# Performance work log

Measured on AMD Instinct MI355X. Metric: run time of the kernel, lower is better.

Reference implementation:

```python
import jax, jax.numpy as jnp
import numpy as np

H, W = 512, 512
N = H * W
NCLS = 4
D_BI, D_SP = 5, 2
THETA_ALPHA, THETA_BETA, THETA_GAMMA = 80.0, 0.0625, 3.0
BI_COMPAT, SP_COMPAT, COMPATIBILITY = 10.0, 3.0, -1.0
NUM_ITER = 10


def _build_lattice(feats):
    """Permutohedral lattice precompute (numpy, integer index construction).
    feats: [N, d]. Returns os [N,d+1] int32 (1-based), ws [N,d+1] float32,
    bn [d+1, M, 2] int32 (0 = missing neighbor), M."""
    feats = np.asarray(feats, np.float64)
    n, d = feats.shape
    inv_std = np.sqrt(2.0 / 3.0) * (d + 1)
    scale = inv_std / np.sqrt((np.arange(d) + 1.0) * (np.arange(d) + 2.0))
    cf = feats * scale
    # embedding matrix E: elevated = cf @ E.T lies on the hyperplane sum=0
    E = np.zeros((d + 1, d))
    E[0, :] = 1.0
    for j in range(1, d + 1):
        E[j, j:] = 1.0
        E[j, j - 1] = -j
    elevated = cf @ E.T  # [n, d+1]
    greedy = (np.rint(elevated / (d + 1)) * (d + 1)).astype(np.int64)
    diff = elevated - greedy
    idx = np.arange(d + 1)
    upper = idx[None, :] > idx[:, None]
    lower = idx[None, :] < idx[:, None]
    di = diff[:, :, None]
    dj = diff[:, None, :]
    rank = (((dj > di) & upper) | ((dj >= di) & lower)).sum(-1)
    rank = rank + greedy.sum(1, keepdims=True) // (d + 1)
    low = rank < 0
    rank = rank + np.where(low, d + 1, 0)
    greedy = greedy + np.where(low, d + 1, 0)
    high = rank > d
    rank = rank - np.where(high, d + 1, 0)
    greedy = greedy - np.where(high, d + 1, 0)
    # barycentric weights
    bary = np.zeros((n, d + 2))
    v = (elevated - greedy) / (d + 1)
    rows = np.repeat(np.arange(n), d + 1)
    np.add.at(bary, (rows, (d - rank).ravel()), v.ravel())
    np.add.at(bary, (rows, (d + 1 - rank).ravel()), -v.ravel())
    bary[:, 0] += 1.0 + bary[:, d + 1]
    ws = bary[:, : d + 1].astype(np.float32)
    # simplex vertex keys (first d coords; last is implied by zero-sum)
    keys = np.empty((n, d + 1, d), np.int64)
    for r in range(d + 1):
        keys[:, r, :] = (greedy + r - (d + 1) * (rank > d - r))[:, :d]
    flat = keys.reshape(-1, d)
    lo = flat.min(0) - (d + 1)
    hi = flat.max(0) + (d + 1)
    strides = np.cumprod(np.concatenate([[1], (hi - lo + 1)[:-1]]))
    coords = (flat - lo) @ strides
    uniq, first, inv = np.unique(coords, return_index=True, return_inverse=True)
    M = int(len(uniq))
    os_ = (inv.reshape(n, d + 1) + 1).astype(np.int32)
    ukeys = flat[first]
    bn = np.zeros((d + 1, M, 2), np.int32)
    for j in range(d + 1):
        n1 = ukeys - 1
        n2 = ukeys + 1
        if j < d:
            n1[:, j] = ukeys[:, j] + d
            n2[:, j] = ukeys[:, j] - d
        for t, nk in enumerate((n1, n2)):
            c = (nk - lo) @ strides
            pos = np.clip(np.searchsorted(uniq, c), 0, M - 1)
            bn[j, :, t] = np.where(uniq[pos] == c, pos + 1, 0)
    return os_, ws, bn, M


def setup_inputs() -> dict:
    key = jax.random.key(0)
    k1, k2 = jax.random.split(key)
    image = jax.random.uniform(k1, (H, W, 7), dtype=jnp.float32)
    unary = jax.random.normal(k2, (H, W, NCLS), dtype=jnp.float32)
    img = np.asarray(image)
    yy, xx = np.mgrid[0:H, 0:W].astype(np.float64)
    bifeat = np.concatenate(
        [(xx / THETA_ALPHA)[..., None], (yy / THETA_ALPHA)[..., None],
         img[..., :3] / THETA_BETA], axis=-1).reshape(N, D_BI)
    spfeat = np.stack([xx / THETA_GAMMA, yy / THETA_GAMMA], -1).reshape(N, D_SP)
    os_b, ws_b, bn_b, M_b = _build_lattice(bifeat)
    os_s, ws_s, bn_s, M_s = _build_lattice(spfeat)
    return {
        "unary": unary,
        "ws_bilateral": jnp.asarray(ws_b), "os_bilateral": jnp.asarray(os_b),
        "blur_neighbors_bilateral": jnp.asarray(bn_b), "M_bilateral": M_b,
        "ws_spatial": jnp.asarray(ws_s), "os_spatial": jnp.asarray(os_s),
        "blur_neighbors_spatial": jnp.asarray(bn_s), "M_spatial": M_s,
    }


def _perm_filter(values, os_, ws, bn, M, alpha):
    # values: [N, C]; splat -> blur -> slice
    d1 = os_.shape[1]
    C = values.shape[1]
    table = jnp.zeros((M + 1, C), values.dtype)  # row 0 = dummy (missing)
    table = table.at[os_.reshape(-1)].add(
        (values[:, None, :] * ws[:, :, None]).reshape(-1, C))
    for j in range(d1):  # [0.5, 1, 0.5] blur along each lattice axis
        table = table.at[1:].add(0.5 * (table[bn[j, :, 0]] + table[bn[j, :, 1]]))
    return alpha * jnp.einsum("nrc,nr->nc", table[os_], ws)


def _mean_field(unary, ws_b, os_b, bn_b, M_b, ws_s, os_s, bn_s, M_s):
    C = unary.shape[-1]
    u = unary.reshape(N, C)
    alpha_b = 1.0 / (1.0 + 2.0 ** (-D_BI))
    alpha_s = 1.0 / (1.0 + 2.0 ** (-D_SP))
    ones = jnp.ones((N, 1), u.dtype)
    inv_nb = 1.0 / (_perm_filter(ones, os_b, ws_b, bn_b, M_b, alpha_b) + 1e-20)
    inv_ns = 1.0 / (_perm_filter(ones, os_s, ws_s, bn_s, M_s, alpha_s) + 1e-20)
    Q = jax.nn.softmax(-u, axis=-1)
    for _ in range(NUM_ITER):
        msg = (BI_COMPAT * _perm_filter(Q, os_b, ws_b, bn_b, M_b, alpha_b) * inv_nb
               + SP_COMPAT * _perm_filter(Q, os_s, ws_s, bn_s, M_s, alpha_s) * inv_ns)
        Q = jax.nn.softmax(-u - COMPATIBILITY * msg, axis=-1)
    return Q.reshape(H, W, C)


def reference(unary, ws_bilateral, os_bilateral, blur_neighbors_bilateral, M_bilateral,
              ws_spatial, os_spatial, blur_neighbors_spatial, M_spatial):
    # Returns the refined marginals Q [H, W, NCLS]; the module's MAP output is
    # jnp.argmax(Q, -1) (kept soft here so fwd/bwd share one output).
    return _mean_field(unary, ws_bilateral, os_bilateral, blur_neighbors_bilateral,
                       M_bilateral, ws_spatial, os_spatial, blur_neighbors_spatial,
                       M_spatial)
```

## Files before the change

kernel.cpp:

```cpp
#include <hip/hip_runtime.h>

#define NPIX (512 * 512)
#define BLK 256

#define TOTB (NPIX * 6)
#define TOTS (NPIX * 3)
#define TOTE (NPIX * 9)

typedef _Float16 h4 __attribute__((ext_vector_type(4)));
typedef unsigned long long u64;

constexpr float ALPHA_B = 32.0f / 33.0f;
constexpr float ALPHA_S = 0.8f;
constexpr float BI_COMPAT = 10.0f;
constexpr float SP_COMPAT = 3.0f;

__device__ __forceinline__ unsigned pack_ent(int n, float w) {
    float wc = fminf(fmaxf(w, 0.f), 1.f);
    unsigned iw = (unsigned)(wc * 16383.f + 0.5f);
    return (iw << 18) | (unsigned)n;
}
__device__ __forceinline__ int ent_pix(unsigned e) { return (int)(e & 0x3FFFFu); }
__device__ __forceinline__ float ent_w(unsigned e) {
    return (float)(e >> 18) * (1.0f / 16383.0f);
}
__device__ __forceinline__ u64 mknode(int nxt, unsigned pay) {
    return ((u64)(unsigned)nxt << 32) | (u64)pay;
}

__device__ __forceinline__ float4 f4zero() { return make_float4(0.f, 0.f, 0.f, 0.f); }
__device__ __forceinline__ h4 h4zero() {
    h4 z; z.x = (_Float16)0.f; z.y = (_Float16)0.f; z.z = (_Float16)0.f; z.w = (_Float16)0.f;
    return z;
}

__global__ void k_softmax_init(const float4* __restrict__ u, float4* __restrict__ Q) {
    int n = blockIdx.x * BLK + threadIdx.x;
    if (n >= NPIX) return;
    float4 uu = u[n];
    float l0 = -uu.x, l1 = -uu.y, l2 = -uu.z, l3 = -uu.w;
    float m = fmaxf(fmaxf(l0, l1), fmaxf(l2, l3));
    float e0 = expf(l0 - m), e1 = expf(l1 - m), e2 = expf(l2 - m), e3 = expf(l3 - m);
    float inv = 1.0f / (e0 + e1 + e2 + e3);
    Q[n] = make_float4(e0 * inv, e1 * inv, e2 * inv, e3 * inv);
}

template <int D1>
__device__ __forceinline__ void link_slot(const int* __restrict__ os, const float* __restrict__ ws,
                                          int* __restrict__ head, u64* __restrict__ next2,
                                          int n, int r, int obase, int ebase, int lane) {
    int o = obase + os[n * D1 + r];
    int e = ebase + n * D1 + r;
    unsigned pay = pack_ent(n, ws[n * D1 + r]);
    int o_prev = __shfl_up(o, 1);
    bool is_head = (lane == 0) || (o != o_prev);
    u64 hm = __ballot(is_head);
    u64 above = (hm >> lane) >> 1;
    int runlen = above ? __ffsll((long long)above) : (64 - lane);
    int e_prevlane = __shfl_up(e, 1);
    u64 node;
    if (is_head) {
        int e_last = e + (runlen - 1) * D1;
        int old = atomicExch(&head[o], e_last);
        node = mknode(old, pay);
    } else {
        node = mknode(e_prevlane, pay);
    }
    next2[e] = node;
}

__global__ void k_link2_softmax(const int* __restrict__ osb, const float* __restrict__ wsb,
                                const int* __restrict__ oss, const float* __restrict__ wss,
                                int* __restrict__ head, u64* __restrict__ next2,
                                const float4* __restrict__ u, float4* __restrict__ Q,
                                int Vb) {
    int n = blockIdx.x * BLK + threadIdx.x;
    float4 uu = u[n];
    float l0 = -uu.x, l1 = -uu.y, l2 = -uu.z, l3 = -uu.w;
    float m = fmaxf(fmaxf(l0, l1), fmaxf(l2, l3));
    float e0 = expf(l0 - m), e1 = expf(l1 - m), e2 = expf(l2 - m), e3 = expf(l3 - m);
    float inv = 1.0f / (e0 + e1 + e2 + e3);
    Q[n] = make_float4(e0 * inv, e1 * inv, e2 * inv, e3 * inv);
    int lane = threadIdx.x & 63;
#pragma unroll
    for (int r = 0; r < 6; r++) link_slot<6>(osb, wsb, head, next2, n, r, 0, 0, lane);
#pragma unroll
    for (int r = 0; r < 3; r++) link_slot<3>(oss, wss, head, next2, n, r, Vb, TOTB, lane);
}

__global__ void k_compact2(const int* __restrict__ head, const u64* __restrict__ next2,
                           unsigned* __restrict__ ent, int* __restrict__ start,
                           int* __restrict__ endv,
                           float* __restrict__ nB, float* __restrict__ nS,
                           int* __restrict__ cursor, int V, int Vb) {
    __shared__ int lds[BLK];
    __shared__ int sbase;
    int o = blockIdx.x * BLK + threadIdx.x;
    bool valid = o < V;
    int h = valid ? head[o] : -1;
    int len = 0;
    for (int e = h; e >= 0;) { e = (int)(next2[e] >> 32); len++; }
    lds[threadIdx.x] = len;
    __syncthreads();
    for (int off = 1; off < BLK; off <<= 1) {
        int t = ((int)threadIdx.x >= off) ? lds[threadIdx.x - off] : 0;
        __syncthreads();
        lds[threadIdx.x] += t;
        __syncthreads();
    }
    int incl = lds[threadIdx.x];
    if (threadIdx.x == BLK - 1) sbase = atomicAdd(cursor, incl);
    __syncthreads();
    if (!valid) return;
    int pos = sbase + incl - len;
    start[o] = pos;
    endv[o] = pos + len;
    float acc = 0.f;
    for (int e = h; e >= 0;) {
        u64 nd = next2[e];
        unsigned pe = (unsigned)nd;
        acc += ent_w(pe);
        ent[pos++] = pe;
        e = (int)(nd >> 32);
    }
    if (o < Vb) nB[o] = acc;
    else nS[o - Vb] = acc;
}

__global__ void k_link_softmax(const int* __restrict__ osb, const int* __restrict__ oss,
                               int* __restrict__ head, int* __restrict__ next,
                               const float4* __restrict__ u, float4* __restrict__ Q,
                               int Vb) {
    int n = blockIdx.x * BLK + threadIdx.x;
    if (n >= NPIX) return;
    float4 uu = u[n];
    float l0 = -uu.x, l1 = -uu.y, l2 = -uu.z, l3 = -uu.w;
    float m = fmaxf(fmaxf(l0, l1), fmaxf(l2, l3));
    float e0 = expf(l0 - m), e1 = expf(l1 - m), e2 = expf(l2 - m), e3 = expf(l3 - m);
    float inv = 1.0f / (e0 + e1 + e2 + e3);
    Q[n] = make_float4(e0 * inv, e1 * inv, e2 * inv, e3 * inv);
#pragma unroll
    for (int r = 0; r < 6; r++) {
        int o = osb[n * 6 + r];
        int e = n * 6 + r;
        next[e] = atomicExch(&head[o], e);
    }
#pragma unroll
    for (int r = 0; r < 3; r++) {
        int o = Vb + oss[n * 3 + r];
        int e = TOTB + n * 3 + r;
        next[e] = atomicExch(&head[o], e);
    }
}

__global__ void k_compact(const int* __restrict__ head, const int* __restrict__ next,
                          const float* __restrict__ wsb, const float* __restrict__ wss,
                          unsigned* __restrict__ ent, int* __restrict__ start,
                          int* __restrict__ endv,
                          float* __restrict__ nB, float* __restrict__ nS,
                          int* __restrict__ cursor, int V, int Vb) {
    __shared__ int lds[BLK];
    __shared__ int sbase;
    int o = blockIdx.x * BLK + threadIdx.x;
    bool valid = o < V;
    int h = valid ? head[o] : -1;
    int len = 0;
    for (int e = h; e >= 0; e = next[e]) len++;
    lds[threadIdx.x] = len;
    __syncthreads();
    for (int off = 1; off < BLK; off <<= 1) {
        int t = ((int)threadIdx.x >= off) ? lds[threadIdx.x - off] : 0;
        __syncthreads();
        lds[threadIdx.x] += t;
        __syncthreads();
    }
    int incl = lds[threadIdx.x];
    if (threadIdx.x == BLK - 1) sbase = atomicAdd(cursor, incl);
    __syncthreads();
    if (!valid) return;
    int pos = sbase + incl - len;
    start[o] = pos;
    endv[o] = pos + len;
    float acc = 0.f;
    if (o < Vb) {
        for (int e = h; e >= 0; e = next[e]) {
            unsigned n = (unsigned)e / 6u;
            unsigned pe = pack_ent((int)n, wsb[e]);
            acc += ent_w(pe);
            ent[pos++] = pe;
        }
        nB[o] = acc;
    } else {
        for (int e = h; e >= 0; e = next[e]) {
            int ee = e - TOTB;
            unsigned pe = pack_ent(ee / 3, wss[ee]);
            acc += ent_w(pe);
            ent[pos++] = pe;
        }
        nS[o - Vb] = acc;
    }
}

__global__ void k_gather4h_both(const unsigned* __restrict__ ent, const int* __restrict__ start,
                                const int* __restrict__ endv, int V, int Vb,
                                h4* __restrict__ tB, h4* __restrict__ tS,
                                const float4* __restrict__ Q) {
    int i = blockIdx.x * BLK + threadIdx.x;
    if (i >= V) return;
    int s = start[i];
    int e = endv[i];
    float ax = 0.f, ay = 0.f, az = 0.f, aw = 0.f;
    for (int k = s; k < e; k++) {
        unsigned en = ent[k];
        float w = ent_w(en);
        float4 q = Q[ent_pix(en)];
        ax += w * q.x; ay += w * q.y; az += w * q.z; aw += w * q.w;
    }
    h4 h;
    h.x = (_Float16)ax; h.y = (_Float16)ay; h.z = (_Float16)az; h.w = (_Float16)aw;
    if (i < Vb) tB[i] = h;
    else tS[i - Vb] = h;
}

__global__ void k_blur1(const float* __restrict__ in, float* __restrict__ out,
                        const int* __restrict__ bn, int M) {
    int i = blockIdx.x * BLK + threadIdx.x;
    if (i > M) return;
    if (i == 0) { out[0] = 0.f; return; }
    int n1 = bn[(size_t)(i - 1) * 2 + 0];
    int n2 = bn[(size_t)(i - 1) * 2 + 1];
    out[i] = in[i] + 0.5f * (in[n1] + in[n2]);
}

__global__ void k_blur1_both(const float* __restrict__ inB, float* __restrict__ outB,
                             const int* __restrict__ bnB, int Mb,
                             const float* __restrict__ inS, float* __restrict__ outS,
                             const int* __restrict__ bnS, int Ms) {
    int i = blockIdx.x * BLK + threadIdx.x;
    const float* in; float* out; const int* bn; int M, idx;
    if (i <= Mb) { in = inB; out = outB; bn = bnB; M = Mb; idx = i; }
    else {
        idx = i - (Mb + 1);
        if (idx > Ms) return;
        in = inS; out = outS; bn = bnS; M = Ms;
    }
    if (idx == 0) { out[0] = 0.f; return; }
    int n1 = bn[(size_t)(idx - 1) * 2 + 0];
    int n2 = bn[(size_t)(idx - 1) * 2 + 1];
    out[idx] = in[idx] + 0.5f * (in[n1] + in[n2]);
}

__global__ void k_blur4h(const h4* __restrict__ in, h4* __restrict__ out,
                         const int* __restrict__ bn, int M) {
    int i = blockIdx.x * BLK + threadIdx.x;
    if (i > M) return;
    if (i == 0) { out[0] = h4zero(); return; }
    int n1 = bn[(size_t)(i - 1) * 2 + 0];
    int n2 = bn[(size_t)(i - 1) * 2 + 1];
    h4 a = in[i], b = in[n1], c = in[n2];
    h4 o;
    o.x = (_Float16)((float)a.x + 0.5f * ((float)b.x + (float)c.x));
    o.y = (_Float16)((float)a.y + 0.5f * ((float)b.y + (float)c.y));
    o.z = (_Float16)((float)a.z + 0.5f * ((float)b.z + (float)c.z));
    o.w = (_Float16)((float)a.w + 0.5f * ((float)b.w + (float)c.w));
    out[i] = o;
}

__global__ void k_blur4h_both(const h4* __restrict__ inB, h4* __restrict__ outB,
                              const int* __restrict__ bnB, int Mb,
                              const h4* __restrict__ inS, h4* __restrict__ outS,
                              const int* __restrict__ bnS, int Ms) {
    int i = blockIdx.x * BLK + threadIdx.x;
    const h4* in; h4* out; const int* bn; int M, idx;
    if (i <= Mb) { in = inB; out = outB; bn = bnB; M = Mb; idx = i; }
    else {
        idx = i - (Mb + 1);
        if (idx > Ms) return;
        in = inS; out = outS; bn = bnS; M = Ms;
    }
    if (idx == 0) { out[0] = h4zero(); return; }
    int n1 = bn[(size_t)(idx - 1) * 2 + 0];
    int n2 = bn[(size_t)(idx - 1) * 2 + 1];
    h4 a = in[idx], b = in[n1], c = in[n2];
    h4 o;
    o.x = (_Float16)((float)a.x + 0.5f * ((float)b.x + (float)c.x));
    o.y = (_Float16)((float)a.y + 0.5f * ((float)b.y + (float)c.y));
    o.z = (_Float16)((float)a.z + 0.5f * ((float)b.z + (float)c.z));
    o.w = (_Float16)((float)a.w + 0.5f * ((float)b.w + (float)c.w));
    out[idx] = o;
}

__global__ void k_norm_prescale(const float* __restrict__ nTb, const float* __restrict__ wsb,
                                const int* __restrict__ osb,
                                const float* __restrict__ nTs, const float* __restrict__ wss,
                                const int* __restrict__ oss,
                                float* __restrict__ wsbp, float* __restrict__ wssp) {
    int n = blockIdx.x * BLK + threadIdx.x;
    if (n >= NPIX) return;
    float sb = 0.f;
#pragma unroll
    for (int r = 0; r < 6; r++) sb += wsb[n * 6 + r] * nTb[osb[n * 6 + r]];
    float cb = BI_COMPAT * ALPHA_B / (ALPHA_B * sb + 1e-20f);
#pragma unroll
    for (int r = 0; r < 6; r++) wsbp[n * 6 + r] = wsb[n * 6 + r] * cb;
    float ss = 0.f;
#pragma unroll
    for (int r = 0; r < 3; r++) ss += wss[n * 3 + r] * nTs[oss[n * 3 + r]];
    float cs = SP_COMPAT * ALPHA_S / (ALPHA_S * ss + 1e-20f);
#pragma unroll
    for (int r = 0; r < 3; r++) wssp[n * 3 + r] = wss[n * 3 + r] * cs;
}

__global__ void k_slice_combine_h(const float4* __restrict__ u,
                                  const h4* __restrict__ tb, const float* __restrict__ wsbp,
                                  const int* __restrict__ osb,
                                  const h4* __restrict__ ts, const float* __restrict__ wssp,
                                  const int* __restrict__ oss,
                                  float4* __restrict__ Qout) {
    int n = blockIdx.x * BLK + threadIdx.x;
    if (n >= NPIX) return;
    float4 uu = u[n];
    float l0 = -uu.x, l1 = -uu.y, l2 = -uu.z, l3 = -uu.w;
#pragma unroll
    for (int r = 0; r < 6; r++) {
        float w = wsbp[n * 6 + r];
        h4 t = tb[osb[n * 6 + r]];
        l0 += w * (float)t.x; l1 += w * (float)t.y; l2 += w * (float)t.z; l3 += w * (float)t.w;
    }
#pragma unroll
    for (int r = 0; r < 3; r++) {
        float w = wssp[n * 3 + r];
        h4 t = ts[oss[n * 3 + r]];
        l0 += w * (float)t.x; l1 += w * (float)t.y; l2 += w * (float)t.z; l3 += w * (float)t.w;
    }
    float m = fmaxf(fmaxf(l0, l1), fmaxf(l2, l3));
    float e0 = expf(l0 - m), e1 = expf(l1 - m), e2 = expf(l2 - m), e3 = expf(l3 - m);
    float inv = 1.0f / (e0 + e1 + e2 + e3);
    Qout[n] = make_float4(e0 * inv, e1 * inv, e2 * inv, e3 * inv);
}

template <int D1>
__global__ void k_splat1(const float* __restrict__ ws, const int* __restrict__ os,
                         float* __restrict__ table) {
    int n = blockIdx.x * BLK + threadIdx.x;
    if (n >= NPIX) return;
#pragma unroll
    for (int r = 0; r < D1; r++) atomicAdd(&table[os[n * D1 + r]], ws[n * D1 + r]);
}

template <int D1>
__global__ void k_splat4(const float4* __restrict__ Q, const float* __restrict__ ws,
                         const int* __restrict__ os, float* __restrict__ table) {
    int n = blockIdx.x * BLK + threadIdx.x;
    if (n >= NPIX) return;
    float4 q = Q[n];
#pragma unroll
    for (int r = 0; r < D1; r++) {
        float w = ws[n * D1 + r];
        int o = os[n * D1 + r];
        float* t = table + 4 * (size_t)o;
        atomicAdd(t + 0, q.x * w);
        atomicAdd(t + 1, q.y * w);
        atomicAdd(t + 2, q.z * w);
        atomicAdd(t + 3, q.w * w);
    }
}

__global__ void k_blur4(const float4* __restrict__ in, float4* __restrict__ out,
                        const int* __restrict__ bn, int M) {
    int i = blockIdx.x * BLK + threadIdx.x;
    if (i > M) return;
    if (i == 0) { out[0] = f4zero(); return; }
    int n1 = bn[(size_t)(i - 1) * 2 + 0];
    int n2 = bn[(size_t)(i - 1) * 2 + 1];
    float4 a = in[i], b = in[n1], c = in[n2];
    out[i] = make_float4(a.x + 0.5f * (b.x + c.x), a.y + 0.5f * (b.y + c.y),
                         a.z + 0.5f * (b.z + c.z), a.w + 0.5f * (b.w + c.w));
}

template <int D1>
__global__ void k_norm_slice(const float* __restrict__ table, const float* __restrict__ ws,
                             const int* __restrict__ os, float alpha,
                             float* __restrict__ inv_out) {
    int n = blockIdx.x * BLK + threadIdx.x;
    if (n >= NPIX) return;
    float s = 0.f;
#pragma unroll
    for (int r = 0; r < D1; r++) s += ws[n * D1 + r] * table[os[n * D1 + r]];
    inv_out[n] = 1.0f / (alpha * s + 1e-20f);
}

__global__ void k_slice_combine(const float4* __restrict__ u,
                                const float4* __restrict__ tb, const float* __restrict__ wsb,
                                const int* __restrict__ osb,
                                const float4* __restrict__ ts, const float* __restrict__ wss,
                                const int* __restrict__ oss,
                                const float* __restrict__ inv_nb,
                                const float* __restrict__ inv_ns,
                                float4* __restrict__ Qout) {
    int n = blockIdx.x * BLK + threadIdx.x;
    if (n >= NPIX) return;
    float4 ab = f4zero();
#pragma unroll
    for (int r = 0; r < 6; r++) {
        float w = wsb[n * 6 + r];
        float4 t = tb[osb[n * 6 + r]];
        ab.x += w * t.x; ab.y += w * t.y; ab.z += w * t.z; ab.w += w * t.w;
    }
    float4 as = f4zero();
#pragma unroll
    for (int r = 0; r < 3; r++) {
        float w = wss[n * 3 + r];
        float4 t = ts[oss[n * 3 + r]];
        as.x += w * t.x; as.y += w * t.y; as.z += w * t.z; as.w += w * t.w;
    }
    float cb = BI_COMPAT * ALPHA_B * inv_nb[n];
    float cs = SP_COMPAT * ALPHA_S * inv_ns[n];
    float4 uu = u[n];
    float l0 = -uu.x + cb * ab.x + cs * as.x;
    float l1 = -uu.y + cb * ab.y + cs * as.y;
    float l2 = -uu.z + cb * ab.z + cs * as.z;
    float l3 = -uu.w + cb * ab.w + cs * as.w;
    float m = fmaxf(fmaxf(l0, l1), fmaxf(l2, l3));
    float e0 = expf(l0 - m), e1 = expf(l1 - m), e2 = expf(l2 - m), e3 = expf(l3 - m);
    float inv = 1.0f / (e0 + e1 + e2 + e3);
    Qout[n] = make_float4(e0 * inv, e1 * inv, e2 * inv, e3 * inv);
}

extern "C" void kernel_launch(void* const* d_in, const int* in_sizes, int n_in,
                              void* d_out, int out_size, void* d_ws, size_t ws_size,
                              hipStream_t stream) {
    const float* unary = (const float*)d_in[0];
    const float* wsb   = (const float*)d_in[1];
    const int*   osb   = (const int*)d_in[2];
    const int*   bnb   = (const int*)d_in[3];
    const float* wss   = (const float*)d_in[5];
    const int*   oss   = (const int*)d_in[6];
    const int*   bns   = (const int*)d_in[7];
    const int Mb = in_sizes[3] / 12;
    const int Ms = in_sizes[7] / 6;
    const int Vb = Mb + 1, Vs = Ms + 1;
    const int V = Vb + Vs;

    float* Q = (float*)d_out;

    char* p = (char*)d_ws;
    auto alloc = [&](size_t nbytes) -> void* {
        void* r = (void*)p;
        p += (nbytes + 15) & ~(size_t)15;
        return r;
    };
    char* region0 = p;
    float* wsbp = (float*)alloc((size_t)NPIX * 6 * 4);
    float* wssp = (float*)alloc((size_t)NPIX * 3 * 4);
    h4*   tAb  = (h4*)alloc((size_t)Vb * 8);
    h4*   tBb  = (h4*)alloc((size_t)Vb * 8);
    h4*   tAs  = (h4*)alloc((size_t)Vs * 8);
    h4*   tBs  = (h4*)alloc((size_t)Vs * 8);
    float* nBb = (float*)alloc((size_t)Vb * 4);
    float* nBs = (float*)alloc((size_t)Vs * 4);
    float* nAb = (float*)alloc((size_t)Vb * 4);
    float* nAs = (float*)alloc((size_t)Vs * 4);
    int*  start = (int*)alloc((size_t)V * 4);
    int*  endv  = (int*)alloc((size_t)V * 4);
    int*  head  = (int*)alloc((size_t)V * 4);
    unsigned* ent = (unsigned*)alloc((size_t)TOTE * 4);
    int*  cursor = (int*)alloc(16);
    size_t base_need = (size_t)(p - (char*)d_ws);
    u64*  next2 = (u64*)alloc((size_t)TOTE * 8);
    size_t need8 = (size_t)(p - (char*)d_ws);
    bool use8 = need8 <= ws_size;
    bool use_gather = base_need <= ws_size;
    int*  next4 = (int*)region0;

    dim3 blk(BLK);
    dim3 gN((NPIX + BLK - 1) / BLK);
    dim3 gVb((Vb + BLK - 1) / BLK);
    dim3 gV((V + BLK - 1) / BLK);
    dim3 gVBS((Vb + Vs + 1 + BLK - 1) / BLK);

    if (use_gather) {
        hipMemsetAsync(head, 0xFF, (size_t)V * 4, stream);
        hipMemsetAsync(cursor, 0, 16, stream);
        if (use8) {
            k_link2_softmax<<<gN, blk, 0, stream>>>(osb, wsb, oss, wss, head, next2,
                                                    (const float4*)unary, (float4*)Q, Vb);
            k_compact2<<<gV, blk, 0, stream>>>(head, next2, ent, start, endv,
                                               nAb, nAs, cursor, V, Vb);
        } else {
            k_link_softmax<<<gN, blk, 0, stream>>>(osb, oss, head, next4,
                                                   (const float4*)unary, (float4*)Q, Vb);
            k_compact<<<gV, blk, 0, stream>>>(head, next4, wsb, wss, ent, start, endv,
                                              nAb, nAs, cursor, V, Vb);
        }

        {
            float* a = nAb; float* b = nBb;
            float* as_ = nAs; float* bs_ = nBs;
            for (int j = 0; j < 3; j++) {
                k_blur1_both<<<gVBS, blk, 0, stream>>>(a, b, bnb + (size_t)j * Mb * 2, Mb,
                                                       as_, bs_, bns + (size_t)j * Ms * 2, Ms);
                float* t = a; a = b; b = t;
                t = as_; as_ = bs_; bs_ = t;
            }
            for (int j = 3; j < 6; j++) {
                k_blur1<<<gVb, blk, 0, stream>>>(a, b, bnb + (size_t)j * Mb * 2, Mb);
                float* t = a; a = b; b = t;
            }
            k_norm_prescale<<<gN, blk, 0, stream>>>(a, wsb, osb, as_, wss, oss, wsbp, wssp);
        }

        for (int it = 0; it < 10; it++) {
            k_gather4h_both<<<gV, blk, 0, stream>>>(ent, start, endv, V, Vb, tAb, tAs,
                                                    (const float4*)Q);
            h4* a = tAb; h4* b = tBb;
            h4* as_ = tAs; h4* bs_ = tBs;
            for (int j = 0; j < 3; j++) {
                k_blur4h_both<<<gVBS, blk, 0, stream>>>(a, b, bnb + (size_t)j * Mb * 2, Mb,
                                                        as_, bs_, bns + (size_t)j * Ms * 2, Ms);
                h4* t = a; a = b; b = t;
                t = as_; as_ = bs_; bs_ = t;
            }
            for (int j = 3; j < 6; j++) {
                k_blur4h<<<gVb, blk, 0, stream>>>(a, b, bnb + (size_t)j * Mb * 2, Mb);
                h4* t = a; a = b; b = t;
            }
            k_slice_combine_h<<<gN, blk, 0, stream>>>((const float4*)unary,
                                                      a, wsbp, osb, as_, wssp, oss,
                                                      (float4*)Q);
        }
    } else {
        char* q = (char*)d_ws;
        auto alloc2 = [&](size_t nbytes) -> void* {
            void* r = (void*)q;
            q += (nbytes + 15) & ~(size_t)15;
            return r;
        };
        float* fAb = (float*)alloc2((size_t)Vb * 4 * sizeof(float));
        float* fBb = (float*)alloc2((size_t)Vb * 4 * sizeof(float));
        float* fAs = (float*)alloc2((size_t)Vs * 4 * sizeof(float));
        float* fBs = (float*)alloc2((size_t)Vs * 4 * sizeof(float));
        float* inv_nb = (float*)alloc2(NPIX * sizeof(float));
        float* inv_ns = (float*)alloc2(NPIX * sizeof(float));
        dim3 gMb((Mb + 1 + BLK - 1) / BLK);
        dim3 gMs((Ms + 1 + BLK - 1) / BLK);

        hipMemsetAsync(fAb, 0, (size_t)Vb * sizeof(float), stream);
        k_splat1<6><<<gN, blk, 0, stream>>>(wsb, osb, fAb);
        {
            float* a = fAb; float* b = fBb;
            for (int j = 0; j < 6; j++) {
                k_blur1<<<gMb, blk, 0, stream>>>(a, b, bnb + (size_t)j * Mb * 2, Mb);
                float* t = a; a = b; b = t;
            }
            k_norm_slice<6><<<gN, blk, 0, stream>>>(a, wsb, osb, ALPHA_B, inv_nb);
        }
        hipMemsetAsync(fAs, 0, (size_t)Vs * sizeof(float), stream);
        k_splat1<3><<<gN, blk, 0, stream>>>(wss, oss, fAs);
        {
            float* a = fAs; float* b = fBs;
            for (int j = 0; j < 3; j++) {
                k_blur1<<<gMs, blk, 0, stream>>>(a, b, bns + (size_t)j * Ms * 2, Ms);
                float* t = a; a = b; b = t;
            }
            k_norm_slice<3><<<gN, blk, 0, stream>>>(a, wss, oss, ALPHA_S, inv_ns);
        }
        k_softmax_init<<<gN, blk, 0, stream>>>((const float4*)unary, (float4*)Q);
        for (int it = 0; it < 10; it++) {
            hipMemsetAsync(fAb, 0, (size_t)Vb * 4 * sizeof(float), stream);
            k_splat4<6><<<gN, blk, 0, stream>>>((const float4*)Q, wsb, osb, fAb);
            float* a = fAb; float* b = fBb;
            for (int j = 0; j < 6; j++) {
                k_blur4<<<gMb, blk, 0, stream>>>((const float4*)a, (float4*)b,
                                                 bnb + (size_t)j * Mb * 2, Mb);
                float* t = a; a = b; b = t;
            }
            float* finb = a;
            hipMemsetAsync(fAs, 0, (size_t)Vs * 4 * sizeof(float), stream);
            k_splat4<3><<<gN, blk, 0, stream>>>((const float4*)Q, wss, oss, fAs);
            float* as_ = fAs; float* bs_ = fBs;
            for (int j = 0; j < 3; j++) {
                k_blur4<<<gMs, blk, 0, stream>>>((const float4*)as_, (float4*)bs_,
                                                 bns + (size_t)j * Ms * 2, Ms);
                float* t = as_; as_ = bs_; bs_ = t;
            }
            float* fins = as_;
            k_slice_combine<<<gN, blk, 0, stream>>>((const float4*)unary,
                                                    (const float4*)finb, wsb, osb,
                                                    (const float4*)fins, wss, oss,
                                                    inv_nb, inv_ns, (float4*)Q);
        }
    }
}
```

Before: 927.7 us.

## Compose pairs of lattice blur passes into single 2-step stencils, drop fp16 intermediates

```diff
diff --git a/kernel.cpp b/kernel.cpp
--- a/kernel.cpp
+++ b/kernel.cpp
@@ -7,7 +7,6 @@
 #define TOTS (NPIX * 3)
 #define TOTE (NPIX * 9)
 
-typedef _Float16 h4 __attribute__((ext_vector_type(4)));
 typedef unsigned long long u64;
 
 constexpr float ALPHA_B = 32.0f / 33.0f;
@@ -29,10 +28,6 @@
 }
 
 __device__ __forceinline__ float4 f4zero() { return make_float4(0.f, 0.f, 0.f, 0.f); }
-__device__ __forceinline__ h4 h4zero() {
-    h4 z; z.x = (_Float16)0.f; z.y = (_Float16)0.f; z.z = (_Float16)0.f; z.w = (_Float16)0.f;
-    return z;
-}
 
 __global__ void k_softmax_init(const float4* __restrict__ u, float4* __restrict__ Q) {
     int n = blockIdx.x * BLK + threadIdx.x;
@@ -45,30 +40,6 @@
     Q[n] = make_float4(e0 * inv, e1 * inv, e2 * inv, e3 * inv);
 }
 
-template <int D1>
-__device__ __forceinline__ void link_slot(const int* __restrict__ os, const float* __restrict__ ws,
-                                          int* __restrict__ head, u64* __restrict__ next2,
-                                          int n, int r, int obase, int ebase, int lane) {
-    int o = obase + os[n * D1 + r];
-    int e = ebase + n * D1 + r;
-    unsigned pay = pack_ent(n, ws[n * D1 + r]);
-    int o_prev = __shfl_up(o, 1);
-    bool is_head = (lane == 0) || (o != o_prev);
-    u64 hm = __ballot(is_head);
-    u64 above = (hm >> lane) >> 1;
-    int runlen = above ? __ffsll((long long)above) : (64 - lane);
-    int e_prevlane = __shfl_up(e, 1);
-    u64 node;
-    if (is_head) {
-        int e_last = e + (runlen - 1) * D1;
-        int old = atomicExch(&head[o], e_last);
-        node = mknode(old, pay);
-    } else {
-        node = mknode(e_prevlane, pay);
-    }
-    next2[e] = node;
-}
-
 __global__ void k_link2_softmax(const int* __restrict__ osb, const float* __restrict__ wsb,
                                 const int* __restrict__ oss, const float* __restrict__ wss,
                                 int* __restrict__ head, u64* __restrict__ next2,
@@ -81,11 +52,20 @@
     float e0 = expf(l0 - m), e1 = expf(l1 - m), e2 = expf(l2 - m), e3 = expf(l3 - m);
     float inv = 1.0f / (e0 + e1 + e2 + e3);
     Q[n] = make_float4(e0 * inv, e1 * inv, e2 * inv, e3 * inv);
-    int lane = threadIdx.x & 63;
-#pragma unroll
-    for (int r = 0; r < 6; r++) link_slot<6>(osb, wsb, head, next2, n, r, 0, 0, lane);
-#pragma unroll
-    for (int r = 0; r < 3; r++) link_slot<3>(oss, wss, head, next2, n, r, Vb, TOTB, lane);
+#pragma unroll
+    for (int r = 0; r < 6; r++) {
+        int o = osb[n * 6 + r];
+        int e = n * 6 + r;
+        int old = atomicExch(&head[o], e);
+        next2[e] = mknode(old, pack_ent(n, wsb[n * 6 + r]));
+    }
+#pragma unroll
+    for (int r = 0; r < 3; r++) {
+        int o = Vb + oss[n * 3 + r];
+        int e = TOTB + n * 3 + r;
+        int old = atomicExch(&head[o], e);
+        next2[e] = mknode(old, pack_ent(n, wss[n * 3 + r]));
+    }
 }
 
 __global__ void k_compact2(const int* __restrict__ head, const u64* __restrict__ next2,
@@ -201,9 +181,134 @@
     }
 }
 
-__global__ void k_gather4h_both(const unsigned* __restrict__ ent, const int* __restrict__ start,
+__global__ void k_compose(const int* __restrict__ bnb, int Mb, int Vb,
+                          const int* __restrict__ bns, int Ms, int Vs,
+                          int* __restrict__ cidxB, int* __restrict__ cidxS) {
+    int t = blockIdx.x * BLK + threadIdx.x;
+    int TB = 3 * Vb;
+    const int* bnj; const int* bnk; int* c; int i, V;
+    if (t < TB) {
+        int p = t / Vb;
+        i = t - p * Vb;
+        if (i == 0) return;
+        bnj = bnb + (size_t)(2 * p) * Mb * 2;
+        bnk = bnb + (size_t)(2 * p + 1) * Mb * 2;
+        c = cidxB + (size_t)p * 8 * Vb;
+        V = Vb;
+    } else {
+        i = t - TB;
+        if (i >= Vs || i == 0) return;
+        bnj = bns;
+        bnk = bns + (size_t)Ms * 2;
+        c = cidxS;
+        V = Vs;
+    }
+    int A = bnk[(size_t)(i - 1) * 2 + 0];
+    int B = bnk[(size_t)(i - 1) * 2 + 1];
+    int a1 = bnj[(size_t)(i - 1) * 2 + 0];
+    int a2 = bnj[(size_t)(i - 1) * 2 + 1];
+    int A1 = 0, A2 = 0, B1 = 0, B2 = 0;
+    if (A > 0) { A1 = bnj[(size_t)(A - 1) * 2 + 0]; A2 = bnj[(size_t)(A - 1) * 2 + 1]; }
+    if (B > 0) { B1 = bnj[(size_t)(B - 1) * 2 + 0]; B2 = bnj[(size_t)(B - 1) * 2 + 1]; }
+    c[0 * (size_t)V + i] = a1;
+    c[1 * (size_t)V + i] = a2;
+    c[2 * (size_t)V + i] = A;
+    c[3 * (size_t)V + i] = A1;
+    c[4 * (size_t)V + i] = A2;
+    c[5 * (size_t)V + i] = B;
+    c[6 * (size_t)V + i] = B1;
+    c[7 * (size_t)V + i] = B2;
+}
+
+__device__ __forceinline__ void blur2f4_core(const float4* __restrict__ in, float4* __restrict__ out,
+                                             const int* __restrict__ c, int V, int i) {
+    if (i == 0) { out[0] = f4zero(); return; }
+    int a1 = c[0 * (size_t)V + i], a2 = c[1 * (size_t)V + i];
+    int A  = c[2 * (size_t)V + i], A1 = c[3 * (size_t)V + i], A2 = c[4 * (size_t)V + i];
+    int B  = c[5 * (size_t)V + i], B1 = c[6 * (size_t)V + i], B2 = c[7 * (size_t)V + i];
+    float4 vi = in[i], va1 = in[a1], va2 = in[a2];
+    float4 vA = in[A], vA1 = in[A1], vA2 = in[A2];
+    float4 vB = in[B], vB1 = in[B1], vB2 = in[B2];
+    float4 o;
+    o.x = vi.x + 0.5f * (va1.x + va2.x + vA.x + vB.x) + 0.25f * (vA1.x + vA2.x + vB1.x + vB2.x);
+    o.y = vi.y + 0.5f * (va1.y + va2.y + vA.y + vB.y) + 0.25f * (vA1.y + vA2.y + vB1.y + vB2.y);
+    o.z = vi.z + 0.5f * (va1.z + va2.z + vA.z + vB.z) + 0.25f * (vA1.z + vA2.z + vB1.z + vB2.z);
+    o.w = vi.w + 0.5f * (va1.w + va2.w + vA.w + vB.w) + 0.25f * (vA1.w + vA2.w + vB1.w + vB2.w);
+    out[i] = o;
+}
+
+__device__ __forceinline__ void blur2f_core(const float* __restrict__ in, float* __restrict__ out,
+                                            const int* __restrict__ c, int V, int i) {
+    if (i == 0) { out[0] = 0.f; return; }
+    int a1 = c[0 * (size_t)V + i], a2 = c[1 * (size_t)V + i];
+    int A  = c[2 * (size_t)V + i], A1 = c[3 * (size_t)V + i], A2 = c[4 * (size_t)V + i];
+    int B  = c[5 * (size_t)V + i], B1 = c[6 * (size_t)V + i], B2 = c[7 * (size_t)V + i];
+    out[i] = in[i] + 0.5f * (in[a1] + in[a2] + in[A] + in[B])
+                   + 0.25f * (in[A1] + in[A2] + in[B1] + in[B2]);
+}
+
+__device__ __forceinline__ void blur1f4_core(const float4* __restrict__ in, float4* __restrict__ out,
+                                             const int* __restrict__ bn, int i) {
+    if (i == 0) { out[0] = f4zero(); return; }
+    int n1 = bn[(size_t)(i - 1) * 2 + 0];
+    int n2 = bn[(size_t)(i - 1) * 2 + 1];
+    float4 a = in[i], b = in[n1], c = in[n2];
+    out[i] = make_float4(a.x + 0.5f * (b.x + c.x), a.y + 0.5f * (b.y + c.y),
+                         a.z + 0.5f * (b.z + c.z), a.w + 0.5f * (b.w + c.w));
+}
+
+__global__ void k_blur2f4_both(const float4* __restrict__ inB, float4* __restrict__ outB,
+                               const int* __restrict__ cB, int Vb,
+                               const float4* __restrict__ inS, float4* __restrict__ outS,
+                               const int* __restrict__ cS, int Vs) {
+    int i = blockIdx.x * BLK + threadIdx.x;
+    if (i < Vb) blur2f4_core(inB, outB, cB, Vb, i);
+    else if (i - Vb < Vs) blur2f4_core(inS, outS, cS, Vs, i - Vb);
+}
+__global__ void k_blur2f4_b1s(const float4* __restrict__ inB, float4* __restrict__ outB,
+                              const int* __restrict__ cB, int Vb,
+                              const float4* __restrict__ inS, float4* __restrict__ outS,
+                              const int* __restrict__ bnS, int Vs) {
+    int i = blockIdx.x * BLK + threadIdx.x;
+    if (i < Vb) blur2f4_core(inB, outB, cB, Vb, i);
+    else if (i - Vb < Vs) blur1f4_core(inS, outS, bnS, i - Vb);
+}
+__global__ void k_blur2f4_b(const float4* __restrict__ inB, float4* __restrict__ outB,
+                            const int* __restrict__ cB, int Vb) {
+    int i = blockIdx.x * BLK + threadIdx.x;
+    if (i < Vb) blur2f4_core(inB, outB, cB, Vb, i);
+}
+__global__ void k_blur2f_both(const float* __restrict__ inB, float* __restrict__ outB,
+                              const int* __restrict__ cB, int Vb,
+                              const float* __restrict__ inS, float* __restrict__ outS,
+                              const int* __restrict__ cS, int Vs) {
+    int i = blockIdx.x * BLK + threadIdx.x;
+    if (i < Vb) blur2f_core(inB, outB, cB, Vb, i);
+    else if (i - Vb < Vs) blur2f_core(inS, outS, cS, Vs, i - Vb);
+}
+__global__ void k_blur2f_b1s(const float* __restrict__ inB, float* __restrict__ outB,
+                             const int* __restrict__ cB, int Vb,
+                             const float* __restrict__ inS, float* __restrict__ outS,
+                             const int* __restrict__ bnS, int Vs) {
+    int i = blockIdx.x * BLK + threadIdx.x;
+    if (i < Vb) blur2f_core(inB, outB, cB, Vb, i);
+    else if (i - Vb < Vs) {
+        int idx = i - Vb;
+        if (idx == 0) { outS[0] = 0.f; return; }
+        int n1 = bnS[(size_t)(idx - 1) * 2 + 0];
+        int n2 = bnS[(size_t)(idx - 1) * 2 + 1];
+        outS[idx] = inS[idx] + 0.5f * (inS[n1] + inS[n2]);
+    }
+}
+__global__ void k_blur2f_b(const float* __restrict__ inB, float* __restrict__ outB,
+                           const int* __restrict__ cB, int Vb) {
+    int i = blockIdx.x * BLK + threadIdx.x;
+    if (i < Vb) blur2f_core(inB, outB, cB, Vb, i);
+}
+
+__global__ void k_gather4f_both(const unsigned* __restrict__ ent, const int* __restrict__ start,
                                 const int* __restrict__ endv, int V, int Vb,
-                                h4* __restrict__ tB, h4* __restrict__ tS,
+                                float4* __restrict__ tB, float4* __restrict__ tS,
                                 const float4* __restrict__ Q) {
     int i = blockIdx.x * BLK + threadIdx.x;
     if (i >= V) return;
@@ -216,8 +321,7 @@
         float4 q = Q[ent_pix(en)];
         ax += w * q.x; ay += w * q.y; az += w * q.z; aw += w * q.w;
     }
-    h4 h;
-    h.x = (_Float16)ax; h.y = (_Float16)ay; h.z = (_Float16)az; h.w = (_Float16)aw;
+    float4 h = make_float4(ax, ay, az, aw);
     if (i < Vb) tB[i] = h;
     else tS[i - Vb] = h;
 }
@@ -250,44 +354,20 @@
     out[idx] = in[idx] + 0.5f * (in[n1] + in[n2]);
 }
 
-__global__ void k_blur4h(const h4* __restrict__ in, h4* __restrict__ out,
-                         const int* __restrict__ bn, int M) {
+__global__ void k_blur4(const float4* __restrict__ in, float4* __restrict__ out,
+                        const int* __restrict__ bn, int M) {
     int i = blockIdx.x * BLK + threadIdx.x;
     if (i > M) return;
-    if (i == 0) { out[0] = h4zero(); return; }
-    int n1 = bn[(size_t)(i - 1) * 2 + 0];
-    int n2 = bn[(size_t)(i - 1) * 2 + 1];
-    h4 a = in[i], b = in[n1], c = in[n2];
-    h4 o;
-    o.x = (_Float16)((float)a.x + 0.5f * ((float)b.x + (float)c.x));
-    o.y = (_Float16)((float)a.y + 0.5f * ((float)b.y + (float)c.y));
-    o.z = (_Float16)((float)a.z + 0.5f * ((float)b.z + (float)c.z));
-    o.w = (_Float16)((float)a.w + 0.5f * ((float)b.w + (float)c.w));
-    out[i] = o;
-}
-
-__global__ void k_blur4h_both(const h4* __restrict__ inB, h4* __restrict__ outB,
-                              const int* __restrict__ bnB, int Mb,
-                              const h4* __restrict__ inS, h4* __restrict__ outS,
-                              const int* __restrict__ bnS, int Ms) {
-    int i = blockIdx.x * BLK + threadIdx.x;
-    const h4* in; h4* out; const int* bn; int M, idx;
-    if (i <= Mb) { in = inB; out = outB; bn = bnB; M = Mb; idx = i; }
-    else {
-        idx = i - (Mb + 1);
-        if (idx > Ms) return;
-        in = inS; out = outS; bn = bnS; M = Ms;
-    }
-    if (idx == 0) { out[0] = h4zero(); return; }
-    int n1 = bn[(size_t)(idx - 1) * 2 + 0];
-    int n2 = bn[(size_t)(idx - 1) * 2 + 1];
-    h4 a = in[idx], b = in[n1], c = in[n2];
-    h4 o;
-    o.x = (_Float16)((float)a.x + 0.5f * ((float)b.x + (float)c.x));
-    o.y = (_Float16)((float)a.y + 0.5f * ((float)b.y + (float)c.y));
-    o.z = (_Float16)((float)a.z + 0.5f * ((float)b.z + (float)c.z));
-    o.w = (_Float16)((float)a.w + 0.5f * ((float)b.w + (float)c.w));
-    out[idx] = o;
+    blur1f4_core(in, out, bn, i);
+}
+
+__global__ void k_blur4_both(const float4* __restrict__ inB, float4* __restrict__ outB,
+                             const int* __restrict__ bnB, int Mb,
+                             const float4* __restrict__ inS, float4* __restrict__ outS,
+                             const int* __restrict__ bnS, int Ms) {
+    int i = blockIdx.x * BLK + threadIdx.x;
+    if (i <= Mb) blur1f4_core(inB, outB, bnB, i);
+    else if (i - (Mb + 1) <= Ms) blur1f4_core(inS, outS, bnS, i - (Mb + 1));
 }
 
 __global__ void k_norm_prescale(const float* __restrict__ nTb, const float* __restrict__ wsb,
@@ -311,10 +391,10 @@
     for (int r = 0; r < 3; r++) wssp[n * 3 + r] = wss[n * 3 + r] * cs;
 }
 
-__global__ void k_slice_combine_h(const float4* __restrict__ u,
-                                  const h4* __restrict__ tb, const float* __restrict__ wsbp,
+__global__ void k_slice_combine_f(const float4* __restrict__ u,
+                                  const float4* __restrict__ tb, const float* __restrict__ wsbp,
                                   const int* __restrict__ osb,
-                                  const h4* __restrict__ ts, const float* __restrict__ wssp,
+                                  const float4* __restrict__ ts, const float* __restrict__ wssp,
                                   const int* __restrict__ oss,
                                   float4* __restrict__ Qout) {
     int n = blockIdx.x * BLK + threadIdx.x;
@@ -324,14 +404,14 @@
 #pragma unroll
     for (int r = 0; r < 6; r++) {
         float w = wsbp[n * 6 + r];
-        h4 t = tb[osb[n * 6 + r]];
-        l0 += w * (float)t.x; l1 += w * (float)t.y; l2 += w * (float)t.z; l3 += w * (float)t.w;
+        float4 t = tb[osb[n * 6 + r]];
+        l0 += w * t.x; l1 += w * t.y; l2 += w * t.z; l3 += w * t.w;
     }
 #pragma unroll
     for (int r = 0; r < 3; r++) {
         float w = wssp[n * 3 + r];
-        h4 t = ts[oss[n * 3 + r]];
-        l0 += w * (float)t.x; l1 += w * (float)t.y; l2 += w * (float)t.z; l3 += w * (float)t.w;
+        float4 t = ts[oss[n * 3 + r]];
+        l0 += w * t.x; l1 += w * t.y; l2 += w * t.z; l3 += w * t.w;
     }
     float m = fmaxf(fmaxf(l0, l1), fmaxf(l2, l3));
     float e0 = expf(l0 - m), e1 = expf(l1 - m), e2 = expf(l2 - m), e3 = expf(l3 - m);
@@ -364,18 +444,6 @@
         atomicAdd(t + 2, q.z * w);
         atomicAdd(t + 3, q.w * w);
     }
-}
-
-__global__ void k_blur4(const float4* __restrict__ in, float4* __restrict__ out,
-                        const int* __restrict__ bn, int M) {
-    int i = blockIdx.x * BLK + threadIdx.x;
-    if (i > M) return;
-    if (i == 0) { out[0] = f4zero(); return; }
-    int n1 = bn[(size_t)(i - 1) * 2 + 0];
-    int n2 = bn[(size_t)(i - 1) * 2 + 1];
-    float4 a = in[i], b = in[n1], c = in[n2];
-    out[i] = make_float4(a.x + 0.5f * (b.x + c.x), a.y + 0.5f * (b.y + c.y),
-                         a.z + 0.5f * (b.z + c.z), a.w + 0.5f * (b.w + c.w));
 }
 
 template <int D1>
@@ -453,10 +521,10 @@
     char* region0 = p;
     float* wsbp = (float*)alloc((size_t)NPIX * 6 * 4);
     float* wssp = (float*)alloc((size_t)NPIX * 3 * 4);
-    h4*   tAb  = (h4*)alloc((size_t)Vb * 8);
-    h4*   tBb  = (h4*)alloc((size_t)Vb * 8);
-    h4*   tAs  = (h4*)alloc((size_t)Vs * 8);
-    h4*   tBs  = (h4*)alloc((size_t)Vs * 8);
+    float4* tAb = (float4*)alloc((size_t)Vb * 16);
+    float4* tBb = (float4*)alloc((size_t)Vb * 16);
+    float4* tAs = (float4*)alloc((size_t)Vs * 16);
+    float4* tBs = (float4*)alloc((size_t)Vs * 16);
     float* nBb = (float*)alloc((size_t)Vb * 4);
     float* nBs = (float*)alloc((size_t)Vs * 4);
     float* nAb = (float*)alloc((size_t)Vb * 4);
@@ -469,19 +537,26 @@
     size_t base_need = (size_t)(p - (char*)d_ws);
     u64*  next2 = (u64*)alloc((size_t)TOTE * 8);
     size_t need8 = (size_t)(p - (char*)d_ws);
+    int* cidxB = (int*)alloc((size_t)Vb * 8 * 3 * 4);
+    int* cidxS = (int*)alloc((size_t)Vs * 8 * 4);
+    size_t need_fused = (size_t)(p - (char*)d_ws);
+    bool use_gather = base_need <= ws_size;
     bool use8 = need8 <= ws_size;
-    bool use_gather = base_need <= ws_size;
+    bool use_fused = need_fused <= ws_size;
     int*  next4 = (int*)region0;
 
     dim3 blk(BLK);
     dim3 gN((NPIX + BLK - 1) / BLK);
     dim3 gVb((Vb + BLK - 1) / BLK);
     dim3 gV((V + BLK - 1) / BLK);
-    dim3 gVBS((Vb + Vs + 1 + BLK - 1) / BLK);
+    dim3 gVBS((Vb + Vs + BLK - 1) / BLK);
+    dim3 gC((3 * Vb + Vs + BLK - 1) / BLK);
 
     if (use_gather) {
         hipMemsetAsync(head, 0xFF, (size_t)V * 4, stream);
         hipMemsetAsync(cursor, 0, 16, stream);
+        if (use_fused)
+            k_compose<<<gC, blk, 0, stream>>>(bnb, Mb, Vb, bns, Ms, Vs, cidxB, cidxS);
         if (use8) {
             k_link2_softmax<<<gN, blk, 0, stream>>>(osb, wsb, oss, wss, head, next2,
                                                     (const float4*)unary, (float4*)Q, Vb);
@@ -494,7 +569,17 @@
                                               nAb, nAs, cursor, V, Vb);
         }
 
-        {
+        const int* cB01 = cidxB;
+        const int* cB23 = cidxB + (size_t)1 * 8 * Vb;
+        const int* cB45 = cidxB + (size_t)2 * 8 * Vb;
+        const int* bnS2 = bns + (size_t)2 * Ms * 2;
+
+        if (use_fused) {
+            k_blur2f_both<<<gVBS, blk, 0, stream>>>(nAb, nBb, cB01, Vb, nAs, nBs, cidxS, Vs);
+            k_blur2f_b1s<<<gVBS, blk, 0, stream>>>(nBb, nAb, cB23, Vb, nBs, nAs, bnS2, Vs);
+            k_blur2f_b<<<gVb, blk, 0, stream>>>(nAb, nBb, cB45, Vb);
+            k_norm_prescale<<<gN, blk, 0, stream>>>(nBb, wsb, osb, nAs, wss, oss, wsbp, wssp);
+        } else {
             float* a = nAb; float* b = nBb;
             float* as_ = nAs; float* bs_ = nBs;
             for (int j = 0; j < 3; j++) {
@@ -511,23 +596,32 @@
         }
 
         for (int it = 0; it < 10; it++) {
-            k_gather4h_both<<<gV, blk, 0, stream>>>(ent, start, endv, V, Vb, tAb, tAs,
+            k_gather4f_both<<<gV, blk, 0, stream>>>(ent, start, endv, V, Vb, tAb, tAs,
                                                     (const float4*)Q);
-            h4* a = tAb; h4* b = tBb;
-            h4* as_ = tAs; h4* bs_ = tBs;
-            for (int j = 0; j < 3; j++) {
-                k_blur4h_both<<<gVBS, blk, 0, stream>>>(a, b, bnb + (size_t)j * Mb * 2, Mb,
-                                                        as_, bs_, bns + (size_t)j * Ms * 2, Ms);
-                h4* t = a; a = b; b = t;
-                t = as_; as_ = bs_; bs_ = t;
+            if (use_fused) {
+                k_blur2f4_both<<<gVBS, blk, 0, stream>>>(tAb, tBb, cB01, Vb, tAs, tBs, cidxS, Vs);
+                k_blur2f4_b1s<<<gVBS, blk, 0, stream>>>(tBb, tAb, cB23, Vb, tBs, tAs, bnS2, Vs);
+                k_blur2f4_b<<<gVb, blk, 0, stream>>>(tAb, tBb, cB45, Vb);
+                k_slice_combine_f<<<gN, blk, 0, stream>>>((const float4*)unary,
+                                                          tBb, wsbp, osb, tAs, wssp, oss,
+                                                          (float4*)Q);
+            } else {
+                float4* a = tAb; float4* b = tBb;
+                float4* as_ = tAs; float4* bs_ = tBs;
+                for (int j = 0; j < 3; j++) {
+                    k_blur4_both<<<gVBS, blk, 0, stream>>>(a, b, bnb + (size_t)j * Mb * 2, Mb,
+                                                           as_, bs_, bns + (size_t)j * Ms * 2, Ms);
+                    float4* t = a; a = b; b = t;
+                    t = as_; as_ = bs_; bs_ = t;
+                }
+                for (int j = 3; j < 6; j++) {
+                    k_blur4<<<gVb, blk, 0, stream>>>(a, b, bnb + (size_t)j * Mb * 2, Mb);
+                    float4* t = a; a = b; b = t;
+                }
+                k_slice_combine_f<<<gN, blk, 0, stream>>>((const float4*)unary,
+                                                          a, wsbp, osb, as_, wssp, oss,
+                                                          (float4*)Q);
             }
-            for (int j = 3; j < 6; j++) {
-                k_blur4h<<<gVb, blk, 0, stream>>>(a, b, bnb + (size_t)j * Mb * 2, Mb);
-                h4* t = a; a = b; b = t;
-            }
-            k_slice_combine_h<<<gN, blk, 0, stream>>>((const float4*)unary,
-                                                      a, wsbp, osb, as_, wssp, oss,
-                                                      (float4*)Q);
         }
     } else {
         char* q = (char*)d_ws;
```

After: 935.5 us. No clear change (+0.8%).
